# Performance work log

Measured on AMD Instinct MI355X. Metric: run time of the kernel, lower is better.

The kernel has to match this reference:

```python
import jax, jax.numpy as jnp
import numpy as np

N = 10000       # num nodes
E = 640000      # num edges (avg degree 64)
D_IN = 128
D_OUT = 128
EPS = 1e-8


def setup_inputs() -> dict:
    key = jax.random.key(0)
    k_x, k_e, k_wm, k_bm, k_wu, k_bu = jax.random.split(key, 6)
    x = jax.random.normal(k_x, (N, D_IN), dtype=jnp.float32)
    edge_index = jax.random.randint(k_e, (2, E), 0, N, dtype=jnp.int32)
    # nn.Linear params (stored as [out, in], applied as x @ W.T + b)
    s_in = 1.0 / np.sqrt(D_IN)
    s_out = 1.0 / np.sqrt(D_OUT)
    W_msg = jax.random.uniform(k_wm, (D_OUT, D_IN), jnp.float32, -s_in, s_in)
    b_msg = jax.random.uniform(k_bm, (D_OUT,), jnp.float32, -s_in, s_in)
    W_upd = jax.random.uniform(k_wu, (D_OUT, D_OUT), jnp.float32, -s_out, s_out)
    b_upd = jax.random.uniform(k_bu, (D_OUT,), jnp.float32, -s_out, s_out)
    return {"x": x, "edge_index": edge_index, "W_msg": W_msg, "b_msg": b_msg,
            "W_upd": W_upd, "b_upd": b_upd}


def reference(x, edge_index, W_msg, b_msg, W_upd, b_upd):
    row, col = edge_index[0], edge_index[1]
    # gather source-node features -> message linear transform: [E, D_OUT]
    messages = x[col] @ W_msg.T + b_msg
    # mean aggregation onto destination nodes (scatter_add + count + divide)
    out = jax.ops.segment_sum(messages, row, num_segments=N)           # [N, D_OUT]
    count = jax.ops.segment_sum(jnp.ones((E,), x.dtype), row, num_segments=N)
    out = out / (count[:, None] + EPS)
    # node update linear transform
    out = out @ W_upd.T + b_upd
    # manifold.project: projective (row-wise) normalization
    out = out / (jnp.linalg.norm(out, axis=-1, keepdims=True) + EPS)
    return out
```

## Files before the change

### kernel.cpp

```cpp
#include <hip/hip_runtime.h>
#include <hip/hip_bf16.h>

#define D 128
#define RPB 8
#define NBMAX 1280
#define EPB 8192
#define CAP 1024
#define OVFCAP 65536
#define EPS 1e-8f

typedef unsigned int uint32;
typedef unsigned short uint16;

__device__ __forceinline__ uint32 f2bf_rne(float f) {
    uint32 u = __float_as_uint(f);
    return (u + 0x7fffu + ((u >> 16) & 1u)) >> 16;
}
__device__ __forceinline__ float bfl(uint32 u) { return __uint_as_float(u << 16); }
__device__ __forceinline__ float bfh(uint32 u) { return __uint_as_float(u & 0xffff0000u); }


__global__ __launch_bounds__(256) void k_zero(int* __restrict__ bcur, int n) {
    int i = blockIdx.x * 256 + threadIdx.x;
    if (i < n) bcur[i] = 0;
}


__global__ __launch_bounds__(512) void k_stage(
        const float* __restrict__ x, const int* __restrict__ ei,
        const float* __restrict__ Wm, const float* __restrict__ Wu,
        uint32* __restrict__ xb, uint32* __restrict__ WTmb, uint32* __restrict__ WTub,
        int* __restrict__ bcur, int* __restrict__ ovfn, uint32* __restrict__ ovf,
        uint32* __restrict__ eb, int E_, int NX, int NB, int nchunk) {
    const int tid = threadIdx.x;

    if (blockIdx.x >= nchunk) {
        int i = (blockIdx.x - nchunk) * 512 + tid;
        if (i < NX) {
            int c = i >> 6, j = i & 63;
            float lo = x[c * D + j];
            float hi = x[c * D + j + 64];
            xb[i] = f2bf_rne(lo) | (f2bf_rne(hi) << 16);
        }
        if (i < 64 * D) {
            int k2 = i >> 7, f = i & 127;
            WTmb[i] = f2bf_rne(Wm[f * D + 2 * k2]) | (f2bf_rne(Wm[f * D + 2 * k2 + 1]) << 16);
            WTub[i] = f2bf_rne(Wu[f * D + 2 * k2]) | (f2bf_rne(Wu[f * D + 2 * k2 + 1]) << 16);
        }
        return;
    }

    __shared__ int h[NBMAX];
    __shared__ int off[NBMAX];
    __shared__ int bias[NBMAX];
    __shared__ uint32 stg[EPB];

    const int base = blockIdx.x * EPB;
    const int nE = min(EPB, E_ - base);

    for (int i = tid; i < NB; i += 512) h[i] = 0;
    __syncthreads();

    for (int i = tid; i < nE; i += 512)
        atomicAdd(&h[ei[base + i] >> 3], 1);
    __syncthreads();

    if (tid < 64) {
        int b0 = tid * 20;
        int loc[20];
        int lsum = 0;
        #pragma unroll
        for (int j = 0; j < 20; ++j) {
            int b = b0 + j;
            int v = (b < NB) ? h[b] : 0;
            loc[j] = lsum;
            lsum += v;
        }
        int run = lsum;
        #pragma unroll
        for (int o = 1; o < 64; o <<= 1) {
            int u = __shfl_up(run, o);
            if (tid >= o) run += u;
        }
        int excl = run - lsum;
        #pragma unroll
        for (int j = 0; j < 20; ++j) {
            int b = b0 + j;
            if (b < NB) off[b] = excl + loc[j];
        }
    }
    __syncthreads();

    for (int b = tid; b < NB; b += 512) {
        int c = h[b];
        if (c) {
            int g = atomicAdd(&bcur[b], c);
            bias[b] = (b << 10) + g - off[b];
        }
    }
    __syncthreads();

    for (int i = tid; i < nE; i += 512) {
        int r = ei[base + i];
        int c = ei[E_ + base + i];
        int b = r >> 3;
        int p = atomicAdd(&off[b], 1);
        stg[p] = ((uint32)r << 16) | (uint32)c;
    }
    __syncthreads();

    for (int i = tid; i < nE; i += 512) {
        uint32 v = stg[i];
        int b = v >> 19;
        int p = bias[b] + i;
        if (p - (b << 10) < CAP) {
            eb[p] = v;
        } else {
            int o = atomicAdd(ovfn, 1);
            if (o < OVFCAP) ovf[o] = v;
        }
    }
}


__global__ __launch_bounds__(256) void k_fused(
        const uint32* __restrict__ xb, const int* __restrict__ bcur,
        const uint32* __restrict__ eb,
        const int* __restrict__ ovfn, const uint32* __restrict__ ovf,
        const uint32* __restrict__ WTmb, const float* __restrict__ bm,
        const uint32* __restrict__ WTub, const float* __restrict__ bu,
        float* __restrict__ out, int N_) {
    __shared__ float a_lds[RPB][D];
    __shared__ float o_lds[RPB][D];
    __shared__ float p_lds[4][RPB][D];
    __shared__ int hist8[RPB], cur8[RPB], rst[RPB], dcnt[RPB];

    uint32* ebl = (uint32*)p_lds;
    uint16* stg = (uint16*)(ebl + CAP);

    const int tid  = threadIdx.x;
    const int lane = tid & 63;
    const int wv   = tid >> 6;

    for (int i = tid; i < RPB * D; i += 256) ((float*)a_lds)[i] = 0.f;
    if (tid < RPB) { hist8[tid] = 0; cur8[tid] = 0; }
    __syncthreads();

    const int ebase = blockIdx.x << 10;
    const int cnt   = bcur[blockIdx.x];
    const int cntc  = min(cnt, CAP);

    {
        int cnt_loc = 0;
        for (int i0 = 0; i0 < cntc; i0 += 256) {
            int i = i0 + tid;
            bool valid = i < cntc;
            uint32 v = valid ? eb[ebase + i] : 0u;
            if (valid) ebl[i] = v;
            int myr = (v >> 16) & 7;
            #pragma unroll
            for (int r = 0; r < RPB; ++r) {
                unsigned long long m = __ballot(valid && (myr == r));
                if (lane == r) cnt_loc += __popcll(m);
            }
        }
        if (lane < RPB && cnt_loc) atomicAdd(&hist8[lane], cnt_loc);
    }
    __syncthreads();
    if (tid == 0) {
        int run = 0;
        #pragma unroll
        for (int r = 0; r < RPB; ++r) { rst[r] = run; run += hist8[r]; dcnt[r] = hist8[r]; }
    }
    __syncthreads();

    for (int i = tid; i < cntc; i += 256) {
        uint32 v = ebl[i];
        int r = (v >> 16) & 7;
        int p = rst[r] + atomicAdd(&cur8[r], 1);
        stg[p] = (uint16)(v & 0xffffu);
    }
    if (cnt > CAP) {
        int no = min(*ovfn, OVFCAP);
        for (int ii = wv * 64; ii < no; ii += 256) {
            int m = min(64, no - ii);
            uint32 v_l = 0;
            if (lane < m) {
                v_l = ovf[ii + lane];
                if ((v_l >> 19) == (uint32)blockIdx.x)
                    atomicAdd(&dcnt[(v_l >> 16) & 7], 1);
            }
            for (int t = 0; t < m; ++t) {
                uint32 ev = __builtin_amdgcn_readlane(v_l, t);
                if ((ev >> 19) != (uint32)blockIdx.x) continue;
                uint32 v = xb[((ev & 0xffffu) << 6) + lane];
                int r = (ev >> 16) & 7;
                atomicAdd(&a_lds[r][lane],      bfl(v));
                atomicAdd(&a_lds[r][lane + 64], bfh(v));
            }
        }
    }
    __syncthreads();

    const int q  = lane >> 4;
    const int lf = lane & 15;
    const uint4* __restrict__ xb4 = (const uint4*)xb;

    #pragma unroll
    for (int j = 0; j < 2; ++j) {
        int r  = wv * 2 + j;
        int lo = rst[r];
        int n  = hist8[r];
        int nq = n >> 2;

        float4 aL = make_float4(0.f, 0.f, 0.f, 0.f);
        float4 aH = make_float4(0.f, 0.f, 0.f, 0.f);

        int it = 0;
        for (; it + 2 <= nq; it += 2) {
            int cA = stg[lo + 4 * it + q];
            int cB = stg[lo + 4 * (it + 1) + q];
            uint4 vA = xb4[(cA << 4) + lf];
            uint4 vB = xb4[(cB << 4) + lf];
            aL.x += bfl(vA.x); aH.x += bfh(vA.x);
            aL.y += bfl(vA.y); aH.y += bfh(vA.y);
            aL.z += bfl(vA.z); aH.z += bfh(vA.z);
            aL.w += bfl(vA.w); aH.w += bfh(vA.w);
            aL.x += bfl(vB.x); aH.x += bfh(vB.x);
            aL.y += bfl(vB.y); aH.y += bfh(vB.y);
            aL.z += bfl(vB.z); aH.z += bfh(vB.z);
            aL.w += bfl(vB.w); aH.w += bfh(vB.w);
        }
        for (; it < nq; ++it) {
            int c = stg[lo + 4 * it + q];
            uint4 v = xb4[(c << 4) + lf];
            aL.x += bfl(v.x); aH.x += bfh(v.x);
            aL.y += bfl(v.y); aH.y += bfh(v.y);
            aL.z += bfl(v.z); aH.z += bfh(v.z);
            aL.w += bfl(v.w); aH.w += bfh(v.w);
        }
        int rem = n & 3;
        if (q < rem) {
            int c = stg[lo + 4 * nq + q];
            uint4 v = xb4[(c << 4) + lf];
            aL.x += bfl(v.x); aH.x += bfh(v.x);
            aL.y += bfl(v.y); aH.y += bfh(v.y);
            aL.z += bfl(v.z); aH.z += bfh(v.z);
            aL.w += bfl(v.w); aH.w += bfh(v.w);
        }
        aL.x += __shfl_xor(aL.x, 16); aL.x += __shfl_xor(aL.x, 32);
        aL.y += __shfl_xor(aL.y, 16); aL.y += __shfl_xor(aL.y, 32);
        aL.z += __shfl_xor(aL.z, 16); aL.z += __shfl_xor(aL.z, 32);
        aL.w += __shfl_xor(aL.w, 16); aL.w += __shfl_xor(aL.w, 32);
        aH.x += __shfl_xor(aH.x, 16); aH.x += __shfl_xor(aH.x, 32);
        aH.y += __shfl_xor(aH.y, 16); aH.y += __shfl_xor(aH.y, 32);
        aH.z += __shfl_xor(aH.z, 16); aH.z += __shfl_xor(aH.z, 32);
        aH.w += __shfl_xor(aH.w, 16); aH.w += __shfl_xor(aH.w, 32);
        if (q == 0) {
            float4 o0 = *(const float4*)&a_lds[r][4 * lf];
            float4 o1 = *(const float4*)&a_lds[r][4 * lf + 64];
            o0.x += aL.x; o0.y += aL.y; o0.z += aL.z; o0.w += aL.w;
            o1.x += aH.x; o1.y += aH.y; o1.z += aH.z; o1.w += aH.w;
            *(float4*)&a_lds[r][4 * lf]      = o0;
            *(float4*)&a_lds[r][4 * lf + 64] = o1;
        }
    }
    __syncthreads();

    const int f0 = lane, f1 = lane + 64;
    const int k0b = wv * 32;

    float acc0[RPB], acc1[RPB];
    #pragma unroll
    for (int r = 0; r < RPB; ++r) { acc0[r] = 0.f; acc1[r] = 0.f; }

    #pragma unroll
    for (int kk = 0; kk < 32; kk += 4) {
        int k2 = (k0b + kk) >> 1;
        uint32 wm00 = WTmb[k2 * D + f0];
        uint32 wm01 = WTmb[(k2 + 1) * D + f0];
        uint32 wm10 = WTmb[k2 * D + f1];
        uint32 wm11 = WTmb[(k2 + 1) * D + f1];
        float w00l = bfl(wm00), w00h = bfh(wm00), w01l = bfl(wm01), w01h = bfh(wm01);
        float w10l = bfl(wm10), w10h = bfh(wm10), w11l = bfl(wm11), w11h = bfh(wm11);
        #pragma unroll
        for (int r = 0; r < RPB; ++r) {
            float4 a4 = *(const float4*)&a_lds[r][k0b + kk];
            acc0[r] += a4.x * w00l + a4.y * w00h + a4.z * w01l + a4.w * w01h;
            acc1[r] += a4.x * w10l + a4.y * w10h + a4.z * w11l + a4.w * w11h;
        }
    }
    #pragma unroll
    for (int r = 0; r < RPB; ++r) {
        p_lds[wv][r][f0] = acc0[r];
        p_lds[wv][r][f1] = acc1[r];
    }
    __syncthreads();

    {
        int r  = tid >> 5;
        int fq = (tid & 31) * 4;
        float4 s0 = *(const float4*)&p_lds[0][r][fq];
        float4 s1 = *(const float4*)&p_lds[1][r][fq];
        float4 s2 = *(const float4*)&p_lds[2][r][fq];
        float4 s3 = *(const float4*)&p_lds[3][r][fq];
        float cntf = (float)dcnt[r];
        float inv = 1.0f / (cntf + EPS);
        float4 b4 = *(const float4*)&bm[fq];
        float4 o;
        o.x = (s0.x + s1.x + s2.x + s3.x + cntf * b4.x) * inv;
        o.y = (s0.y + s1.y + s2.y + s3.y + cntf * b4.y) * inv;
        o.z = (s0.z + s1.z + s2.z + s3.z + cntf * b4.z) * inv;
        o.w = (s0.w + s1.w + s2.w + s3.w + cntf * b4.w) * inv;
        *(float4*)&o_lds[r][fq] = o;
    }
    __syncthreads();

    #pragma unroll
    for (int r = 0; r < RPB; ++r) { acc0[r] = 0.f; acc1[r] = 0.f; }

    #pragma unroll
    for (int kk = 0; kk < 32; kk += 4) {
        int k2 = (k0b + kk) >> 1;
        uint32 wu00 = WTub[k2 * D + f0];
        uint32 wu01 = WTub[(k2 + 1) * D + f0];
        uint32 wu10 = WTub[k2 * D + f1];
        uint32 wu11 = WTub[(k2 + 1) * D + f1];
        float w00l = bfl(wu00), w00h = bfh(wu00), w01l = bfl(wu01), w01h = bfh(wu01);
        float w10l = bfl(wu10), w10h = bfh(wu10), w11l = bfl(wu11), w11h = bfh(wu11);
        #pragma unroll
        for (int r = 0; r < RPB; ++r) {
            float4 a4 = *(const float4*)&o_lds[r][k0b + kk];
            acc0[r] += a4.x * w00l + a4.y * w00h + a4.z * w01l + a4.w * w01h;
            acc1[r] += a4.x * w10l + a4.y * w10h + a4.z * w11l + a4.w * w11h;
        }
    }
    __syncthreads();
    #pragma unroll
    for (int r = 0; r < RPB; ++r) {
        p_lds[wv][r][f0] = acc0[r];
        p_lds[wv][r][f1] = acc1[r];
    }
    __syncthreads();

    {
        int r  = tid >> 5;
        int fq = (tid & 31) * 4;
        float4 s0 = *(const float4*)&p_lds[0][r][fq];
        float4 s1 = *(const float4*)&p_lds[1][r][fq];
        float4 s2 = *(const float4*)&p_lds[2][r][fq];
        float4 s3 = *(const float4*)&p_lds[3][r][fq];
        float4 b4 = *(const float4*)&bu[fq];
        float4 t;
        t.x = s0.x + s1.x + s2.x + s3.x + b4.x;
        t.y = s0.y + s1.y + s2.y + s3.y + b4.y;
        t.z = s0.z + s1.z + s2.z + s3.z + b4.z;
        t.w = s0.w + s1.w + s2.w + s3.w + b4.w;
        float ss = t.x * t.x + t.y * t.y + t.z * t.z + t.w * t.w;
        #pragma unroll
        for (int o = 16; o > 0; o >>= 1) ss += __shfl_xor(ss, o);
        float scale = 1.0f / (sqrtf(ss) + EPS);
        int n = blockIdx.x * RPB + r;
        if (n < N_) {
            float4 w;
            w.x = t.x * scale; w.y = t.y * scale; w.z = t.z * scale; w.w = t.w * scale;
            ((float4*)out)[n * 32 + (tid & 31)] = w;
        }
    }
}


extern "C" void kernel_launch(void* const* d_in, const int* in_sizes, int n_in,
                              void* d_out, int out_size, void* d_ws, size_t ws_size,
                              hipStream_t stream) {
    const float* x  = (const float*)d_in[0];
    const int*   ei = (const int*)d_in[1];
    const float* Wm = (const float*)d_in[2];
    const float* bm = (const float*)d_in[3];
    const float* Wu = (const float*)d_in[4];
    const float* bu = (const float*)d_in[5];
    float* out = (float*)d_out;

    const int N_ = in_sizes[0] / D;
    const int E_ = in_sizes[1] / 2;
    const int NX = N_ * (D / 2);
    const int NB = (N_ + RPB - 1) / RPB;

    uint32* xb   = (uint32*)d_ws;
    uint32* eb   = xb + NX;
    uint32* WTmb = eb + (size_t)NB * CAP;
    uint32* WTub = WTmb + 64 * D;
    int*    bcur = (int*)(WTub + 64 * D);
    int*    ovfn = bcur + NB;
    uint32* ovf  = (uint32*)(ovfn + 1);

    k_zero<<<(NB + 1 + 255) / 256, 256, 0, stream>>>(bcur, NB + 1);

    const int nchunk = (E_ + EPB - 1) / EPB;
    const int npack  = (NX + 511) / 512;
    k_stage<<<nchunk + npack, 512, 0, stream>>>(
        x, ei, Wm, Wu, xb, WTmb, WTub, bcur, ovfn, ovf, eb, E_, NX, NB, nchunk);

    k_fused<<<NB, 256, 0, stream>>>(xb, bcur, eb, ovfn, ovf,
                                    WTmb, bm, WTub, bu, out, N_);
}
```

Baseline: 51.09 us.

## Double rows per block to 16 and widen fused kernel to 512 threads

Raises the number of destination nodes per block from 8 to 16, so the bucket index, capacity and edge packing change and the fused kernel runs with 512 threads across 8 waves. The two small matmuls are split so each half of the waves handles 8 rows, which halves how often each block reloads the weight matrices. The gather loop is unrolled to four outstanding row loads per iteration. In exchange the block count drops to about 625, which lowers parallelism across CUs, and LDS use per block grows.

```diff
diff --git a/kernel.cpp b/kernel.cpp
--- a/kernel.cpp
+++ b/kernel.cpp
@@ -2,10 +2,10 @@
 #include <hip/hip_bf16.h>
 
 #define D 128
-#define RPB 8
-#define NBMAX 1280
+#define RPB 16
+#define NBMAX 640
 #define EPB 8192
-#define CAP 1024
+#define CAP 2048
 #define OVFCAP 65536
 #define EPS 1e-8f
 
@@ -62,15 +62,15 @@
     __syncthreads();
 
     for (int i = tid; i < nE; i += 512)
-        atomicAdd(&h[ei[base + i] >> 3], 1);
+        atomicAdd(&h[ei[base + i] >> 4], 1);
     __syncthreads();
 
     if (tid < 64) {
-        int b0 = tid * 20;
-        int loc[20];
+        int b0 = tid * 10;
+        int loc[10];
         int lsum = 0;
         #pragma unroll
-        for (int j = 0; j < 20; ++j) {
+        for (int j = 0; j < 10; ++j) {
             int b = b0 + j;
             int v = (b < NB) ? h[b] : 0;
             loc[j] = lsum;
@@ -84,7 +84,7 @@
         }
         int excl = run - lsum;
         #pragma unroll
-        for (int j = 0; j < 20; ++j) {
+        for (int j = 0; j < 10; ++j) {
             int b = b0 + j;
             if (b < NB) off[b] = excl + loc[j];
         }
@@ -95,7 +95,7 @@
         int c = h[b];
         if (c) {
             int g = atomicAdd(&bcur[b], c);
-            bias[b] = (b << 10) + g - off[b];
+            bias[b] = (b << 11) + g - off[b];
         }
     }
     __syncthreads();
@@ -103,7 +103,7 @@
     for (int i = tid; i < nE; i += 512) {
         int r = ei[base + i];
         int c = ei[E_ + base + i];
-        int b = r >> 3;
+        int b = r >> 4;
         int p = atomicAdd(&off[b], 1);
         stg[p] = ((uint32)r << 16) | (uint32)c;
     }
@@ -111,9 +111,9 @@
 
     for (int i = tid; i < nE; i += 512) {
         uint32 v = stg[i];
-        int b = v >> 19;
+        int b = v >> 20;
         int p = bias[b] + i;
-        if (p - (b << 10) < CAP) {
+        if (p - (b << 11) < CAP) {
             eb[p] = v;
         } else {
             int o = atomicAdd(ovfn, 1);
@@ -123,7 +123,7 @@
 }
 
 
-__global__ __launch_bounds__(256) void k_fused(
+__global__ __launch_bounds__(512) void k_fused(
         const uint32* __restrict__ xb, const int* __restrict__ bcur,
         const uint32* __restrict__ eb,
         const int* __restrict__ ovfn, const uint32* __restrict__ ovf,
@@ -132,8 +132,8 @@
         float* __restrict__ out, int N_) {
     __shared__ float a_lds[RPB][D];
     __shared__ float o_lds[RPB][D];
-    __shared__ float p_lds[4][RPB][D];
-    __shared__ int hist8[RPB], cur8[RPB], rst[RPB], dcnt[RPB];
+    __shared__ float p_lds[8][RPB / 2][D];
+    __shared__ int hist16[RPB], cur16[RPB], rst[RPB], dcnt[RPB];
 
     uint32* ebl = (uint32*)p_lds;
     uint16* stg = (uint16*)(ebl + CAP);
@@ -142,59 +142,59 @@
     const int lane = tid & 63;
     const int wv   = tid >> 6;
 
-    for (int i = tid; i < RPB * D; i += 256) ((float*)a_lds)[i] = 0.f;
-    if (tid < RPB) { hist8[tid] = 0; cur8[tid] = 0; }
-    __syncthreads();
-
-    const int ebase = blockIdx.x << 10;
+    for (int i = tid; i < RPB * D; i += 512) ((float*)a_lds)[i] = 0.f;
+    if (tid < RPB) { hist16[tid] = 0; cur16[tid] = 0; }
+    __syncthreads();
+
+    const int ebase = blockIdx.x << 11;
     const int cnt   = bcur[blockIdx.x];
     const int cntc  = min(cnt, CAP);
 
     {
         int cnt_loc = 0;
-        for (int i0 = 0; i0 < cntc; i0 += 256) {
+        for (int i0 = 0; i0 < cntc; i0 += 512) {
             int i = i0 + tid;
             bool valid = i < cntc;
             uint32 v = valid ? eb[ebase + i] : 0u;
             if (valid) ebl[i] = v;
-            int myr = (v >> 16) & 7;
+            int myr = (v >> 16) & 15;
             #pragma unroll
             for (int r = 0; r < RPB; ++r) {
                 unsigned long long m = __ballot(valid && (myr == r));
                 if (lane == r) cnt_loc += __popcll(m);
             }
         }
-        if (lane < RPB && cnt_loc) atomicAdd(&hist8[lane], cnt_loc);
+        if (lane < RPB && cnt_loc) atomicAdd(&hist16[lane], cnt_loc);
     }
     __syncthreads();
     if (tid == 0) {
         int run = 0;
         #pragma unroll
-        for (int r = 0; r < RPB; ++r) { rst[r] = run; run += hist8[r]; dcnt[r] = hist8[r]; }
-    }
-    __syncthreads();
-
-    for (int i = tid; i < cntc; i += 256) {
+        for (int r = 0; r < RPB; ++r) { rst[r] = run; run += hist16[r]; dcnt[r] = hist16[r]; }
+    }
+    __syncthreads();
+
+    for (int i = tid; i < cntc; i += 512) {
         uint32 v = ebl[i];
-        int r = (v >> 16) & 7;
-        int p = rst[r] + atomicAdd(&cur8[r], 1);
+        int r = (v >> 16) & 15;
+        int p = rst[r] + atomicAdd(&cur16[r], 1);
         stg[p] = (uint16)(v & 0xffffu);
     }
     if (cnt > CAP) {
         int no = min(*ovfn, OVFCAP);
-        for (int ii = wv * 64; ii < no; ii += 256) {
+        for (int ii = wv * 64; ii < no; ii += 512) {
             int m = min(64, no - ii);
             uint32 v_l = 0;
             if (lane < m) {
                 v_l = ovf[ii + lane];
-                if ((v_l >> 19) == (uint32)blockIdx.x)
-                    atomicAdd(&dcnt[(v_l >> 16) & 7], 1);
+                if ((v_l >> 20) == (uint32)blockIdx.x)
+                    atomicAdd(&dcnt[(v_l >> 16) & 15], 1);
             }
             for (int t = 0; t < m; ++t) {
                 uint32 ev = __builtin_amdgcn_readlane(v_l, t);
-                if ((ev >> 19) != (uint32)blockIdx.x) continue;
+                if ((ev >> 20) != (uint32)blockIdx.x) continue;
                 uint32 v = xb[((ev & 0xffffu) << 6) + lane];
-                int r = (ev >> 16) & 7;
+                int r = (ev >> 16) & 15;
                 atomicAdd(&a_lds[r][lane],      bfl(v));
                 atomicAdd(&a_lds[r][lane + 64], bfh(v));
             }
@@ -210,18 +210,22 @@
     for (int j = 0; j < 2; ++j) {
         int r  = wv * 2 + j;
         int lo = rst[r];
-        int n  = hist8[r];
+        int n  = hist16[r];
         int nq = n >> 2;
 
         float4 aL = make_float4(0.f, 0.f, 0.f, 0.f);
         float4 aH = make_float4(0.f, 0.f, 0.f, 0.f);
 
         int it = 0;
-        for (; it + 2 <= nq; it += 2) {
+        for (; it + 4 <= nq; it += 4) {
             int cA = stg[lo + 4 * it + q];
             int cB = stg[lo + 4 * (it + 1) + q];
+            int cC = stg[lo + 4 * (it + 2) + q];
+            int cD = stg[lo + 4 * (it + 3) + q];
             uint4 vA = xb4[(cA << 4) + lf];
             uint4 vB = xb4[(cB << 4) + lf];
+            uint4 vC = xb4[(cC << 4) + lf];
+            uint4 vD = xb4[(cD << 4) + lf];
             aL.x += bfl(vA.x); aH.x += bfh(vA.x);
             aL.y += bfl(vA.y); aH.y += bfh(vA.y);
             aL.z += bfl(vA.z); aH.z += bfh(vA.z);
@@ -230,6 +234,14 @@
             aL.y += bfl(vB.y); aH.y += bfh(vB.y);
             aL.z += bfl(vB.z); aH.z += bfh(vB.z);
             aL.w += bfl(vB.w); aH.w += bfh(vB.w);
+            aL.x += bfl(vC.x); aH.x += bfh(vC.x);
+            aL.y += bfl(vC.y); aH.y += bfh(vC.y);
+            aL.z += bfl(vC.z); aH.z += bfh(vC.z);
+            aL.w += bfl(vC.w); aH.w += bfh(vC.w);
+            aL.x += bfl(vD.x); aH.x += bfh(vD.x);
+            aL.y += bfl(vD.y); aH.y += bfh(vD.y);
+            aL.z += bfl(vD.z); aH.z += bfh(vD.z);
+            aL.w += bfl(vD.w); aH.w += bfh(vD.w);
         }
         for (; it < nq; ++it) {
             int c = stg[lo + 4 * it + q];
@@ -268,11 +280,12 @@
     __syncthreads();
 
     const int f0 = lane, f1 = lane + 64;
-    const int k0b = wv * 32;
-
-    float acc0[RPB], acc1[RPB];
-    #pragma unroll
-    for (int r = 0; r < RPB; ++r) { acc0[r] = 0.f; acc1[r] = 0.f; }
+    const int hh  = wv >> 2;
+    const int k0b = (wv & 3) * 32;
+
+    float acc0[8], acc1[8];
+    #pragma unroll
+    for (int r = 0; r < 8; ++r) { acc0[r] = 0.f; acc1[r] = 0.f; }
 
     #pragma unroll
     for (int kk = 0; kk < 32; kk += 4) {
@@ -284,27 +297,29 @@
         float w00l = bfl(wm00), w00h = bfh(wm00), w01l = bfl(wm01), w01h = bfh(wm01);
         float w10l = bfl(wm10), w10h = bfh(wm10), w11l = bfl(wm11), w11h = bfh(wm11);
         #pragma unroll
-        for (int r = 0; r < RPB; ++r) {
-            float4 a4 = *(const float4*)&a_lds[r][k0b + kk];
+        for (int r = 0; r < 8; ++r) {
+            float4 a4 = *(const float4*)&a_lds[hh * 8 + r][k0b + kk];
             acc0[r] += a4.x * w00l + a4.y * w00h + a4.z * w01l + a4.w * w01h;
             acc1[r] += a4.x * w10l + a4.y * w10h + a4.z * w11l + a4.w * w11h;
         }
     }
     #pragma unroll
-    for (int r = 0; r < RPB; ++r) {
+    for (int r = 0; r < 8; ++r) {
         p_lds[wv][r][f0] = acc0[r];
         p_lds[wv][r][f1] = acc1[r];
     }
     __syncthreads();
 
     {
-        int r  = tid >> 5;
-        int fq = (tid & 31) * 4;
-        float4 s0 = *(const float4*)&p_lds[0][r][fq];
-        float4 s1 = *(const float4*)&p_lds[1][r][fq];
-        float4 s2 = *(const float4*)&p_lds[2][r][fq];
-        float4 s3 = *(const float4*)&p_lds[3][r][fq];
-        float cntf = (float)dcnt[r];
+        int row = tid >> 5;
+        int fq  = (tid & 31) * 4;
+        int pb  = (row >> 3) * 4;
+        int r8  = row & 7;
+        float4 s0 = *(const float4*)&p_lds[pb + 0][r8][fq];
+        float4 s1 = *(const float4*)&p_lds[pb + 1][r8][fq];
+        float4 s2 = *(const float4*)&p_lds[pb + 2][r8][fq];
+        float4 s3 = *(const float4*)&p_lds[pb + 3][r8][fq];
+        float cntf = (float)dcnt[row];
         float inv = 1.0f / (cntf + EPS);
         float4 b4 = *(const float4*)&bm[fq];
         float4 o;
@@ -312,12 +327,12 @@
         o.y = (s0.y + s1.y + s2.y + s3.y + cntf * b4.y) * inv;
         o.z = (s0.z + s1.z + s2.z + s3.z + cntf * b4.z) * inv;
         o.w = (s0.w + s1.w + s2.w + s3.w + cntf * b4.w) * inv;
-        *(float4*)&o_lds[r][fq] = o;
-    }
-    __syncthreads();
-
-    #pragma unroll
-    for (int r = 0; r < RPB; ++r) { acc0[r] = 0.f; acc1[r] = 0.f; }
+        *(float4*)&o_lds[row][fq] = o;
+    }
+    __syncthreads();
+
+    #pragma unroll
+    for (int r = 0; r < 8; ++r) { acc0[r] = 0.f; acc1[r] = 0.f; }
 
     #pragma unroll
     for (int kk = 0; kk < 32; kk += 4) {
@@ -329,27 +344,29 @@
         float w00l = bfl(wu00), w00h = bfh(wu00), w01l = bfl(wu01), w01h = bfh(wu01);
         float w10l = bfl(wu10), w10h = bfh(wu10), w11l = bfl(wu11), w11h = bfh(wu11);
         #pragma unroll
-        for (int r = 0; r < RPB; ++r) {
-            float4 a4 = *(const float4*)&o_lds[r][k0b + kk];
+        for (int r = 0; r < 8; ++r) {
+            float4 a4 = *(const float4*)&o_lds[hh * 8 + r][k0b + kk];
             acc0[r] += a4.x * w00l + a4.y * w00h + a4.z * w01l + a4.w * w01h;
             acc1[r] += a4.x * w10l + a4.y * w10h + a4.z * w11l + a4.w * w11h;
         }
     }
     __syncthreads();
     #pragma unroll
-    for (int r = 0; r < RPB; ++r) {
+    for (int r = 0; r < 8; ++r) {
         p_lds[wv][r][f0] = acc0[r];
         p_lds[wv][r][f1] = acc1[r];
     }
     __syncthreads();
 
     {
-        int r  = tid >> 5;
-        int fq = (tid & 31) * 4;
-        float4 s0 = *(const float4*)&p_lds[0][r][fq];
-        float4 s1 = *(const float4*)&p_lds[1][r][fq];
-        float4 s2 = *(const float4*)&p_lds[2][r][fq];
-        float4 s3 = *(const float4*)&p_lds[3][r][fq];
+        int row = tid >> 5;
+        int fq  = (tid & 31) * 4;
+        int pb  = (row >> 3) * 4;
+        int r8  = row & 7;
+        float4 s0 = *(const float4*)&p_lds[pb + 0][r8][fq];
+        float4 s1 = *(const float4*)&p_lds[pb + 1][r8][fq];
+        float4 s2 = *(const float4*)&p_lds[pb + 2][r8][fq];
+        float4 s3 = *(const float4*)&p_lds[pb + 3][r8][fq];
         float4 b4 = *(const float4*)&bu[fq];
         float4 t;
         t.x = s0.x + s1.x + s2.x + s3.x + b4.x;
@@ -360,7 +377,7 @@
         #pragma unroll
         for (int o = 16; o > 0; o >>= 1) ss += __shfl_xor(ss, o);
         float scale = 1.0f / (sqrtf(ss) + EPS);
-        int n = blockIdx.x * RPB + r;
+        int n = blockIdx.x * RPB + row;
         if (n < N_) {
             float4 w;
             w.x = t.x * scale; w.y = t.y * scale; w.z = t.z * scale; w.w = t.w * scale;
@@ -401,6 +418,6 @@
     k_stage<<<nchunk + npack, 512, 0, stream>>>(
         x, ei, Wm, Wu, xb, WTmb, WTub, bcur, ovfn, ovf, eb, E_, NX, NB, nchunk);
 
-    k_fused<<<NB, 256, 0, stream>>>(xb, bcur, eb, ovfn, ovf,
+    k_fused<<<NB, 512, 0, stream>>>(xb, bcur, eb, ovfn, ovf,
                                     WTmb, bm, WTub, bu, out, N_);
 }
```

Result: slower. 52.87 us (+3.5%).
